# Kernel tuning notes

Measured on AMD Instinct MI355X. Metric: run time of the kernel, lower is better.

## Reference

```python
import jax, jax.numpy as jnp
import numpy as np

B, T, K = 64, 2000, 256
BLANK_LOGPROB = -1.0
NEG = jnp.float32(-1e30)  # stand-in for -inf, safe under logaddexp


def setup_inputs() -> dict:
    key = jax.random.key(0)
    k1, k2, k3 = jax.random.split(key, 3)
    attn_logprob = jax.random.normal(k1, (B, 1, T, K), dtype=jnp.float32)
    key_lens = jax.random.randint(k2, (B,), K // 2, K + 1)
    query_lens = jax.random.randint(k3, (B,), T // 2, T + 1)
    return {"attn_logprob": attn_logprob, "key_lens": key_lens, "query_lens": query_lens}


def _forward_sum(attn_logprob, key_lens, query_lens):
    # attn_logprob: [B, 1, T, K]; targets are 1..K_b (strictly increasing, all distinct)
    Bn, _, Tn, Kn = attn_logprob.shape
    logp = attn_logprob[:, 0]                                   # [B, T, K]
    # pad blank class at key index 0 (torch F.pad(pad=(1,0), value=blank_logprob))
    padded = jnp.pad(logp, ((0, 0), (0, 0), (1, 0)), constant_values=BLANK_LOGPROB)  # [B,T,K+1]
    # masked log_softmax over classes 0..K_b (matches per-sample slice [:key_lens+1])
    key_idx = jnp.arange(Kn + 1)
    key_mask = key_idx[None, :] <= key_lens[:, None]            # [B, K+1]
    masked = jnp.where(key_mask[:, None, :], padded, NEG)
    log_probs = jax.nn.log_softmax(masked, axis=-1)             # [B, T, K+1]

    # CTC forward DP. States s = 0..2K: even -> blank (class 0), odd -> label (s+1)//2.
    S = 2 * Kn + 1
    s_idx = jnp.arange(S)
    lab = jnp.where(s_idx % 2 == 0, 0, (s_idx + 1) // 2)        # class index per state
    # skip transition s-2 -> s allowed for odd s >= 3 (all labels distinct)
    skip_ok = (s_idx % 2 == 1) & (s_idx >= 3)

    emit0 = log_probs[:, 0, :][:, lab]                          # [B, S]
    alpha0 = jnp.full((Bn, S), NEG, dtype=log_probs.dtype)
    alpha0 = alpha0.at[:, 0].set(emit0[:, 0]).at[:, 1].set(emit0[:, 1])

    xs = jnp.moveaxis(log_probs[:, 1:, :], 1, 0)                # [T-1, B, K+1]
    ts = jnp.arange(1, Tn)

    def step(alpha, inp):
        x, t = inp
        emit = x[:, lab]                                        # [B, S]
        sh1 = jnp.concatenate([jnp.full((Bn, 1), NEG, alpha.dtype), alpha[:, :-1]], axis=1)
        sh2 = jnp.concatenate([jnp.full((Bn, 2), NEG, alpha.dtype), alpha[:, :-2]], axis=1)
        sh2 = jnp.where(skip_ok[None, :], sh2, NEG)
        new = jnp.logaddexp(jnp.logaddexp(alpha, sh1), sh2) + emit
        # freeze alpha once t >= query_lens[b] so final carry = alpha at t = T_b - 1
        return jnp.where((t < query_lens)[:, None], new, alpha), None

    alpha_final, _ = jax.lax.scan(step, alpha0, (xs, ts))       # [B, S]

    last = 2 * key_lens                                          # final state index per sample
    a_last = jnp.take_along_axis(alpha_final, last[:, None], axis=1)[:, 0]
    a_prev = jnp.take_along_axis(alpha_final, (last - 1)[:, None], axis=1)[:, 0]
    nll = -jnp.logaddexp(a_last, a_prev)                         # per-sample CTC NLL
    # torch CTCLoss(reduction='mean') on a batch of 1: divide by target length
    loss = nll / jnp.maximum(key_lens, 1).astype(nll.dtype)
    loss = jnp.where(nll > 0.5e30, 0.0, loss)                    # zero_infinity
    return jnp.mean(loss)


def reference(attn_logprob, key_lens, query_lens):
    return _forward_sum(attn_logprob, key_lens, query_lens)
```

## Files before the change

### kernel.cpp

```cpp
#include <hip/hip_runtime.h>
#include <cstdint>
#include <cstddef>

#define BB    64
#define TB    2000
#define KB    256

constexpr float LOG2E = 1.4426950408889634f;
constexpr float LN2f  = 0.6931471805599453f;
constexpr float WBF   = 0.36787944117144233f;

__device__ __forceinline__ float exp2i(int k) {
  return __uint_as_float((uint32_t)(127 + k) << 23);
}
__device__ __forceinline__ float shr1z(float v) {
  return __int_as_float(__builtin_amdgcn_update_dpp(
      0, __float_as_int(v), 0x138, 0xF, 0xF, true));
}
__device__ __forceinline__ float dmax64(float v) {
#define DSTEP(ctrl, rm, bc)                                                  \
  { float t = __int_as_float(__builtin_amdgcn_update_dpp(                    \
        __float_as_int(v), __float_as_int(v), (ctrl), (rm), 0xF, (bc)));     \
    v = fmaxf(v, t); }
  DSTEP(0x111, 0xF, true) DSTEP(0x112, 0xF, true) DSTEP(0x114, 0xF, true)
  DSTEP(0x118, 0xF, true) DSTEP(0x142, 0xA, false) DSTEP(0x143, 0xC, false)
#undef DSTEP
  return __int_as_float(__builtin_amdgcn_readlane(__float_as_int(v), 63));
}
__device__ __forceinline__ float dsum64(float v) {
#define DSTEP(ctrl, rm, bc)                                                  \
  { float t = __int_as_float(__builtin_amdgcn_update_dpp(                    \
        __float_as_int(v), __float_as_int(v), (ctrl), (rm), 0xF, (bc)));     \
    v += t; }
  DSTEP(0x111, 0xF, true) DSTEP(0x112, 0xF, true) DSTEP(0x114, 0xF, true)
  DSTEP(0x118, 0xF, true) DSTEP(0x142, 0xA, false) DSTEP(0x143, 0xC, false)
#undef DSTEP
  return v;
}
__device__ __forceinline__ float wsum64(float v) {
#pragma unroll
  for (int m = 32; m >= 1; m >>= 1) v += __shfl_xor(v, m, 64);
  return v;
}

__global__ __launch_bounds__(256, 1)
void fsl_main(const float* __restrict__ x, const int* __restrict__ key_lens,
              const int* __restrict__ query_lens, float* __restrict__ partial,
              float* __restrict__ alast, float* __restrict__ aprev) {
  __shared__ __align__(16) char ring[65536];
  __shared__ __align__(16) int prodG[4];
  __shared__ int consG;

  const int tid  = threadIdx.x;
  const int b    = blockIdx.x;
  const int lane = tid & 63;
  const int w    = tid >> 6;
  const int kl   = key_lens[b];
  const int qlen = query_lens[b];
  const int total = qlen - 1;
  const int ng    = (total + 7) >> 3;
  const float* xb  = x + (size_t)b * (TB * KB);
  const char*  xbc = (const char*)xb;
  const int lane16 = lane << 4;

  if (tid == 0) { prodG[0] = 0; prodG[1] = 0; prodG[2] = 0; prodG[3] = 0x7fffffff; consG = 0; }
  __syncthreads();

  if (w == 0) {
    float a0 = 0.f, a1 = 0.f, a2 = 0.f, a3 = 0.f;
    float b0 = 0.f, b1 = 0.f, b2 = 0.f, b3 = 0.f, s512 = 0.f;
    if (lane == 0) { a0 = WBF; b0 = __builtin_amdgcn_exp2f(xb[0] * LOG2E); }
    int Cw = 0;
    float m_red = dmax64(fmaxf(a0, b0));

    float4 e0, e1, e2, e3, e4, e5, e6, e7;
    float4 f0, f1, f2, f3, f4, f5, f6, f7;
    float4 g0, g1, g2, g3, g4, g5, g6, g7;

#define POLL(GN) do {                                                        \
    const int tgt_ = (GN);                                                   \
    for (;;) {                                                               \
      __asm__ __volatile__("" ::: "memory");                                 \
      const int4 fl_ = *(const int4*)prodG;                                  \
      if (min(fl_.x, min(fl_.y, fl_.z)) >= tgt_) break;                      \
      __builtin_amdgcn_s_sleep(1);                                           \
    }                                                                        \
    __asm__ __volatile__("" ::: "memory");                                   \
  } while (0)

#define LD8(E, g) do {                                                       \
    const char* sb_ = ring + (((g) & 7) << 13) + lane16;                     \
    E##0 = *(const float4*)(sb_);                                            \
    E##1 = *(const float4*)(sb_ + 1024);                                     \
    E##2 = *(const float4*)(sb_ + 2048);                                     \
    E##3 = *(const float4*)(sb_ + 3072);                                     \
    E##4 = *(const float4*)(sb_ + 4096);                                     \
    E##5 = *(const float4*)(sb_ + 5120);                                     \
    E##6 = *(const float4*)(sb_ + 6144);                                     \
    E##7 = *(const float4*)(sb_ + 7168);                                     \
  } while (0)

#define STEP1(EV) do {                                                       \
    const float pm1 = shr1z(b3);                                             \
    const float t0_ = a0 + pm1;                                              \
    const float t1_ = a1 + b0;                                               \
    const float t2_ = a2 + b1;                                               \
    const float t3_ = a3 + b2;                                               \
    s512 = s512 + b3;                                                        \
    b0 = (b0 + t0_) * EV.x;                                                  \
    b1 = (b1 + t1_) * EV.y;                                                  \
    b2 = (b2 + t2_) * EV.z;                                                  \
    b3 = (b3 + t3_) * EV.w;                                                  \
    a0 = t0_; a1 = t1_; a2 = t2_; a3 = t3_;                                  \
  } while (0)

#define STEP1G(EV, J) do { if ((J) < rem_) { STEP1(EV); } } while (0)

#define RUN8(E)  do { STEP1(E##0); STEP1(E##1); STEP1(E##2); STEP1(E##3);    \
                      STEP1(E##4); STEP1(E##5); STEP1(E##6); STEP1(E##7); } while (0)
#define RUN8G(E, RM) do { const int rem_ = (RM);                             \
                      STEP1G(E##0,0); STEP1G(E##1,1); STEP1G(E##2,2);        \
                      STEP1G(E##3,3); STEP1G(E##4,4); STEP1G(E##5,5);        \
                      STEP1G(E##6,6); STEP1G(E##7,7); } while (0)

#define APPLY() do {                                                         \
    int e_ = (int)((__float_as_uint(m_red) >> 23) & 0xFF) - 127;             \
    if (!(m_red > 0.f)) e_ = -24;                                            \
    const int k_ = e_ + 24;                      \
    if (k_ > 126) {                                                          \
      const int kh_ = k_ >> 1;                                               \
      const float s1_ = exp2i(-kh_), s2_ = exp2i(-(k_ - kh_));               \
      a0 *= s1_; a1 *= s1_; a2 *= s1_; a3 *= s1_;                            \
      b0 *= s1_; b1 *= s1_; b2 *= s1_; b3 *= s1_; s512 *= s1_;               \
      a0 *= s2_; a1 *= s2_; a2 *= s2_; a3 *= s2_;                            \
      b0 *= s2_; b1 *= s2_; b2 *= s2_; b3 *= s2_; s512 *= s2_;               \
    } else {                                                                 \
      const float s_ = exp2i(-k_);                                           \
      a0 *= s_; a1 *= s_; a2 *= s_; a3 *= s_;                                \
      b0 *= s_; b1 *= s_; b2 *= s_; b3 *= s_; s512 *= s_;                    \
    }                                                                        \
    Cw += k_;                                                                \
  } while (0)

#define MEASURE() do {                                                       \
    float ml_ = fmaxf(fmaxf(fmaxf(a0, a1), fmaxf(a2, a3)),                   \
                      fmaxf(fmaxf(b0, b1), fmaxf(b2, b3)));                  \
    ml_ = fmaxf(ml_, s512);                                                  \
    m_red = dmax64(ml_);                                                     \
  } while (0)

#define RUNGRP(E, G) do {                                                    \
    if (8 * (G) + 8 <= total) { RUN8(E); }                                   \
    else { RUN8G(E, total - 8 * (G)); }                                      \
    APPLY(); MEASURE();                                                      \
  } while (0)

    POLL(3);
    LD8(e, 0);
    if (1 < ng) LD8(f, 1);
    if (2 < ng) LD8(g, 2);
    int cg = 0;
    while (cg + 6 <= ng && 8 * (cg + 3) <= total) {
      POLL(cg + 6);
      RUN8(e); APPLY(); MEASURE(); LD8(e, cg + 3);
      RUN8(f); APPLY(); MEASURE(); LD8(f, cg + 4);
      RUN8(g); APPLY(); MEASURE(); LD8(g, cg + 5);
      __asm__ __volatile__("" ::: "memory");
      if (lane == 0) *(volatile int*)&consG = cg + 6;
      cg += 3;
    }
    for (; cg < ng; cg += 3) {
      POLL(min(cg + 6, ng));
      RUNGRP(e, cg);
      if (cg + 3 < ng) LD8(e, cg + 3);
      if (cg + 1 < ng) {
        RUNGRP(f, cg + 1);
        if (cg + 4 < ng) LD8(f, cg + 4);
      }
      if (cg + 2 < ng) {
        RUNGRP(g, cg + 2);
        if (cg + 5 < ng) LD8(g, cg + 5);
      }
      __asm__ __volatile__("" ::: "memory");
      if (lane == 0) *(volatile int*)&consG = cg + 6;
    }
#undef POLL
#undef LD8
#undef STEP1
#undef STEP1G
#undef RUN8
#undef RUN8G
#undef APPLY
#undef MEASURE
#undef RUNGRP

    float* ev = (float*)ring;
    float* od = (float*)(ring + 4096);
    *(float4*)(ev + (lane << 2)) = make_float4(a0, a1, a2, a3);
    *(float4*)(od + (lane << 2)) = make_float4(b0, b1, b2, b3);
    if (lane == 63) *(float*)(ring + 8192) = s512;
    __asm__ __volatile__("" ::: "memory");
    if (lane == 0) {
      const float aL = (kl < 256) ? ev[kl] : *(float*)(ring + 8192);
      const float aP = od[kl - 1];
      const float dC = (float)Cw - (float)total * LOG2E;
      alast[b] = (log2f(aL) + dC) * LN2f;
      aprev[b] = (log2f(aP) + dC) * LN2f;
    }
  } else {
    const int pw = w - 1;
    const int c0 = lane << 2;
    const float bs0 = (c0 + 0 < kl) ? LOG2E : -20000.f;
    const float bs1 = (c0 + 1 < kl) ? LOG2E : -20000.f;
    const float bs2 = (c0 + 2 < kl) ? LOG2E : -20000.f;
    const float bs3 = (c0 + 3 < kl) ? LOG2E : -20000.f;
    volatile int* vc = &consG;
    float acc = 0.f;

    if (pw == 0) {
      const float4 v = *(const float4*)(xbc + lane16);
      float s_ = __builtin_amdgcn_exp2f(fmaf(v.x, LOG2E, bs0))
               + __builtin_amdgcn_exp2f(fmaf(v.y, LOG2E, bs1))
               + __builtin_amdgcn_exp2f(fmaf(v.z, LOG2E, bs2))
               + __builtin_amdgcn_exp2f(fmaf(v.w, LOG2E, bs3));
      s_ = dsum64(s_);
      acc += __builtin_amdgcn_logf((s_ + 1.0f) * WBF);
    }

    float4 A0, A1, A2, A3, A4, A5, A6, A7;
    float4 B0, B1, B2, B3, B4, B5, B6, B7;
    float4 C0, C1, C2, C3, C4, C5, C6, C7;

#define LOADG(P, GG) do {                                                    \
    const int rb_ = 8 * (GG) + 1;                                            \
    P##0 = *(const float4*)(xbc + (size_t)min(rb_ + 0, TB - 1) * 1024 + lane16); \
    P##1 = *(const float4*)(xbc + (size_t)min(rb_ + 1, TB - 1) * 1024 + lane16); \
    P##2 = *(const float4*)(xbc + (size_t)min(rb_ + 2, TB - 1) * 1024 + lane16); \
    P##3 = *(const float4*)(xbc + (size_t)min(rb_ + 3, TB - 1) * 1024 + lane16); \
    P##4 = *(const float4*)(xbc + (size_t)min(rb_ + 4, TB - 1) * 1024 + lane16); \
    P##5 = *(const float4*)(xbc + (size_t)min(rb_ + 5, TB - 1) * 1024 + lane16); \
    P##6 = *(const float4*)(xbc + (size_t)min(rb_ + 6, TB - 1) * 1024 + lane16); \
    P##7 = *(const float4*)(xbc + (size_t)min(rb_ + 7, TB - 1) * 1024 + lane16); \
  } while (0)

#define PR1(V, J) do {                                                       \
    float4 wv_;                                                              \
    wv_.x = __builtin_amdgcn_exp2f(fmaf(V.x, LOG2E, bs0));                   \
    wv_.y = __builtin_amdgcn_exp2f(fmaf(V.y, LOG2E, bs1));                   \
    wv_.z = __builtin_amdgcn_exp2f(fmaf(V.z, LOG2E, bs2));                   \
    wv_.w = __builtin_amdgcn_exp2f(fmaf(V.w, LOG2E, bs3));                   \
    *(float4*)(dstb_ + ((J) << 10)) = wv_;                                   \
    if (rb_ + (J) <= total) {                                                \
      float sr_ = (wv_.x + wv_.y) + (wv_.z + wv_.w);                         \
      sr_ = dsum64(sr_);                                                     \
      acc += __builtin_amdgcn_logf((sr_ + 1.0f) * WBF);                      \
    }                                                                        \
  } while (0)

#define PROC(P, GG) do {                                                     \
    const int rb_ = 8 * (GG) + 1;                                            \
    if ((GG) >= 8) {                                    \
      int c_ = *vc;                                                          \
      while (c_ < (GG) - 7) { __builtin_amdgcn_s_sleep(2); c_ = *vc; }       \
      __asm__ __volatile__("" ::: "memory");                                 \
    }                                                                        \
    char* dstb_ = ring + (((GG) & 7) << 13) + lane16;                        \
    PR1(P##0, 0); PR1(P##1, 1); PR1(P##2, 2); PR1(P##3, 3);                  \
    PR1(P##4, 4); PR1(P##5, 5); PR1(P##6, 6); PR1(P##7, 7);                  \
    __asm__ __volatile__("s_waitcnt lgkmcnt(0)" ::: "memory");               \
    if (lane == 0) *(volatile int*)&prodG[pw] = (GG) + 3;                    \
  } while (0)

    LOADG(A, pw); LOADG(B, pw + 3);
    int g = pw;
    for (;;) {
      LOADG(C, g + 6);
      PROC(A, g);
      g += 3; if (g >= ng) break;
      LOADG(A, g + 6);
      PROC(B, g);
      g += 3; if (g >= ng) break;
      LOADG(B, g + 6);
      PROC(C, g);
      g += 3; if (g >= ng) break;
    }
#undef LOADG
#undef PR1
#undef PROC
    __asm__ __volatile__("" ::: "memory");
    if (lane == 0) *(volatile int*)&prodG[pw] = 0x7fffffff;
    if (lane == 63) partial[4 * b + pw] = acc;
  }
}

__global__ __launch_bounds__(64)
void fsl_finish(const float* __restrict__ partial, const int* __restrict__ key_lens,
                const float* __restrict__ alast, const float* __restrict__ aprev,
                float* __restrict__ out) {
  const int b = threadIdx.x;
  const float SumLse =
      ((partial[4 * b] + partial[4 * b + 1]) + partial[4 * b + 2]) * LN2f;
  const float al = alast[b], ap = aprev[b];
  const float mx = fmaxf(al, ap);
  const float lae = (mx == -INFINITY) ? -INFINITY
                                      : mx + log1pf(expf(-fabsf(al - ap)));
  const float nll = SumLse - lae;
  const int kl = key_lens[b];
  float lv = nll / (float)max(kl, 1);
  if (nll > 5e29f) lv = 0.f;
  float v = wsum64(lv);
  if (b == 0) out[0] = v * (1.0f / 64.0f);
}

extern "C" void kernel_launch(void* const* d_in, const int* in_sizes, int n_in,
                              void* d_out, int out_size, void* d_ws, size_t ws_size,
                              hipStream_t stream) {
  const float* x     = (const float*)d_in[0];
  const int*   klens = (const int*)d_in[1];
  const int*   qlens = (const int*)d_in[2];
  float* out = (float*)d_out;

  float* partial = (float*)d_ws;
  float* alast   = partial + BB * 4;
  float* aprev   = alast + BB;

  fsl_main  <<<BB, 256, 0, stream>>>(x, klens, qlens, partial, alast, aprev);
  fsl_finish<<<1, 64, 0, stream>>>(partial, klens, alast, aprev, out);
}
```

Measured before the change: 119.7 us.

## Offload per-row log-sum-exp to separate blocks, freeing producer warps for DP feed

Moves the per-timestep log-sum-exp normalizer computation out of the producer warps in the 64 DP blocks and into 2000 extra blocks. Each extra warp handles 16 rows of one sample. The finish kernel now reduces 125 partials per sample. Producer warps only do exp and the LDS write, which shortens the critical path feeding the serial DP warp. The change also removes the sleep in the consumer poll loop and enlarges the shared ring declaration. The extra blocks re-read the whole input from HBM and compete for CUs with the 64 DP blocks; the larger LDS allocation may also limit co-residency.

```diff
diff --git a/kernel.cpp b/kernel.cpp
--- a/kernel.cpp
+++ b/kernel.cpp
@@ -5,6 +5,9 @@
 #define BB    64
 #define TB    2000
 #define KB    256
+#define WPB   125
+#define RPW   16
+#define NLSEB 2000
 
 constexpr float LOG2E = 1.4426950408889634f;
 constexpr float LN2f  = 0.6931471805599453f;
@@ -43,39 +46,44 @@
   return v;
 }
 
+typedef const __attribute__((address_space(1))) unsigned int* gas1p;
+typedef __attribute__((address_space(3))) unsigned int* las3p;
+
 __global__ __launch_bounds__(256, 1)
 void fsl_main(const float* __restrict__ x, const int* __restrict__ key_lens,
               const int* __restrict__ query_lens, float* __restrict__ partial,
               float* __restrict__ alast, float* __restrict__ aprev) {
-  __shared__ __align__(16) char ring[65536];
+  __shared__ __align__(16) char ring[86016];
   __shared__ __align__(16) int prodG[4];
   __shared__ int consG;
 
   const int tid  = threadIdx.x;
-  const int b    = blockIdx.x;
   const int lane = tid & 63;
   const int w    = tid >> 6;
-  const int kl   = key_lens[b];
-  const int qlen = query_lens[b];
-  const int total = qlen - 1;
-  const int ng    = (total + 7) >> 3;
-  const float* xb  = x + (size_t)b * (TB * KB);
-  const char*  xbc = (const char*)xb;
-  const int lane16 = lane << 4;
-
-  if (tid == 0) { prodG[0] = 0; prodG[1] = 0; prodG[2] = 0; prodG[3] = 0x7fffffff; consG = 0; }
-  __syncthreads();
-
-  if (w == 0) {
-    float a0 = 0.f, a1 = 0.f, a2 = 0.f, a3 = 0.f;
-    float b0 = 0.f, b1 = 0.f, b2 = 0.f, b3 = 0.f, s512 = 0.f;
-    if (lane == 0) { a0 = WBF; b0 = __builtin_amdgcn_exp2f(xb[0] * LOG2E); }
-    int Cw = 0;
-    float m_red = dmax64(fmaxf(a0, b0));
-
-    float4 e0, e1, e2, e3, e4, e5, e6, e7;
-    float4 f0, f1, f2, f3, f4, f5, f6, f7;
-    float4 g0, g1, g2, g3, g4, g5, g6, g7;
+
+  if (blockIdx.x < BB) {
+    const int b    = blockIdx.x;
+    const int kl   = key_lens[b];
+    const int qlen = query_lens[b];
+    const int total = qlen - 1;
+    const int ng    = (total + 7) >> 3;
+    const float* xb  = x + (size_t)b * (TB * KB);
+    const char*  xbc = (const char*)xb;
+    const int lane16 = lane << 4;
+
+    if (tid == 0) { prodG[0] = 0; prodG[1] = 0; prodG[2] = 0; prodG[3] = 0x7fffffff; consG = 0; }
+    __syncthreads();
+
+    if (w == 0) {
+      float a0 = 0.f, a1 = 0.f, a2 = 0.f, a3 = 0.f;
+      float b0 = 0.f, b1 = 0.f, b2 = 0.f, b3 = 0.f, s512 = 0.f;
+      if (lane == 0) { a0 = WBF; b0 = __builtin_amdgcn_exp2f(xb[0] * LOG2E); }
+      int Cw = 0;
+      float m_red = dmax64(fmaxf(a0, b0));
+
+      float4 e0, e1, e2, e3, e4, e5, e6, e7;
+      float4 f0, f1, f2, f3, f4, f5, f6, f7;
+      float4 g0, g1, g2, g3, g4, g5, g6, g7;
 
 #define POLL(GN) do {                                                        \
     const int tgt_ = (GN);                                                   \
@@ -83,7 +91,6 @@
       __asm__ __volatile__("" ::: "memory");                                 \
       const int4 fl_ = *(const int4*)prodG;                                  \
       if (min(fl_.x, min(fl_.y, fl_.z)) >= tgt_) break;                      \
-      __builtin_amdgcn_s_sleep(1);                                           \
     }                                                                        \
     __asm__ __volatile__("" ::: "memory");                                   \
   } while (0)
@@ -155,35 +162,35 @@
     APPLY(); MEASURE();                                                      \
   } while (0)
 
-    POLL(3);
-    LD8(e, 0);
-    if (1 < ng) LD8(f, 1);
-    if (2 < ng) LD8(g, 2);
-    int cg = 0;
-    while (cg + 6 <= ng && 8 * (cg + 3) <= total) {
-      POLL(cg + 6);
-      RUN8(e); APPLY(); MEASURE(); LD8(e, cg + 3);
-      RUN8(f); APPLY(); MEASURE(); LD8(f, cg + 4);
-      RUN8(g); APPLY(); MEASURE(); LD8(g, cg + 5);
-      __asm__ __volatile__("" ::: "memory");
-      if (lane == 0) *(volatile int*)&consG = cg + 6;
-      cg += 3;
-    }
-    for (; cg < ng; cg += 3) {
-      POLL(min(cg + 6, ng));
-      RUNGRP(e, cg);
-      if (cg + 3 < ng) LD8(e, cg + 3);
-      if (cg + 1 < ng) {
-        RUNGRP(f, cg + 1);
-        if (cg + 4 < ng) LD8(f, cg + 4);
+      POLL(3);
+      LD8(e, 0);
+      if (1 < ng) LD8(f, 1);
+      if (2 < ng) LD8(g, 2);
+      int cg = 0;
+      while (cg + 6 <= ng && 8 * (cg + 3) <= total) {
+        POLL(cg + 6);
+        RUN8(e); APPLY(); MEASURE(); LD8(e, cg + 3);
+        RUN8(f); APPLY(); MEASURE(); LD8(f, cg + 4);
+        RUN8(g); APPLY(); MEASURE(); LD8(g, cg + 5);
+        __asm__ __volatile__("" ::: "memory");
+        if (lane == 0) *(volatile int*)&consG = cg + 6;
+        cg += 3;
       }
-      if (cg + 2 < ng) {
-        RUNGRP(g, cg + 2);
-        if (cg + 5 < ng) LD8(g, cg + 5);
+      for (; cg < ng; cg += 3) {
+        POLL(min(cg + 6, ng));
+        RUNGRP(e, cg);
+        if (cg + 3 < ng) LD8(e, cg + 3);
+        if (cg + 1 < ng) {
+          RUNGRP(f, cg + 1);
+          if (cg + 4 < ng) LD8(f, cg + 4);
+        }
+        if (cg + 2 < ng) {
+          RUNGRP(g, cg + 2);
+          if (cg + 5 < ng) LD8(g, cg + 5);
+        }
+        __asm__ __volatile__("" ::: "memory");
+        if (lane == 0) *(volatile int*)&consG = cg + 6;
       }
-      __asm__ __volatile__("" ::: "memory");
-      if (lane == 0) *(volatile int*)&consG = cg + 6;
-    }
 #undef POLL
 #undef LD8
 #undef STEP1
@@ -194,42 +201,31 @@
 #undef MEASURE
 #undef RUNGRP
 
-    float* ev = (float*)ring;
-    float* od = (float*)(ring + 4096);
-    *(float4*)(ev + (lane << 2)) = make_float4(a0, a1, a2, a3);
-    *(float4*)(od + (lane << 2)) = make_float4(b0, b1, b2, b3);
-    if (lane == 63) *(float*)(ring + 8192) = s512;
-    __asm__ __volatile__("" ::: "memory");
-    if (lane == 0) {
-      const float aL = (kl < 256) ? ev[kl] : *(float*)(ring + 8192);
-      const float aP = od[kl - 1];
-      const float dC = (float)Cw - (float)total * LOG2E;
-      alast[b] = (log2f(aL) + dC) * LN2f;
-      aprev[b] = (log2f(aP) + dC) * LN2f;
-    }
-  } else {
-    const int pw = w - 1;
-    const int c0 = lane << 2;
-    const float bs0 = (c0 + 0 < kl) ? LOG2E : -20000.f;
-    const float bs1 = (c0 + 1 < kl) ? LOG2E : -20000.f;
-    const float bs2 = (c0 + 2 < kl) ? LOG2E : -20000.f;
-    const float bs3 = (c0 + 3 < kl) ? LOG2E : -20000.f;
-    volatile int* vc = &consG;
-    float acc = 0.f;
-
-    if (pw == 0) {
-      const float4 v = *(const float4*)(xbc + lane16);
-      float s_ = __builtin_amdgcn_exp2f(fmaf(v.x, LOG2E, bs0))
-               + __builtin_amdgcn_exp2f(fmaf(v.y, LOG2E, bs1))
-               + __builtin_amdgcn_exp2f(fmaf(v.z, LOG2E, bs2))
-               + __builtin_amdgcn_exp2f(fmaf(v.w, LOG2E, bs3));
-      s_ = dsum64(s_);
-      acc += __builtin_amdgcn_logf((s_ + 1.0f) * WBF);
-    }
-
-    float4 A0, A1, A2, A3, A4, A5, A6, A7;
-    float4 B0, B1, B2, B3, B4, B5, B6, B7;
-    float4 C0, C1, C2, C3, C4, C5, C6, C7;
+      float* ev = (float*)ring;
+      float* od = (float*)(ring + 4096);
+      *(float4*)(ev + (lane << 2)) = make_float4(a0, a1, a2, a3);
+      *(float4*)(od + (lane << 2)) = make_float4(b0, b1, b2, b3);
+      if (lane == 63) *(float*)(ring + 8192) = s512;
+      __asm__ __volatile__("" ::: "memory");
+      if (lane == 0) {
+        const float aL = (kl < 256) ? ev[kl] : *(float*)(ring + 8192);
+        const float aP = od[kl - 1];
+        const float dC = (float)Cw - (float)total * LOG2E;
+        alast[b] = (log2f(aL) + dC) * LN2f;
+        aprev[b] = (log2f(aP) + dC) * LN2f;
+      }
+    } else {
+      const int pw = w - 1;
+      const int c0 = lane << 2;
+      const float bs0 = (c0 + 0 < kl) ? LOG2E : -20000.f;
+      const float bs1 = (c0 + 1 < kl) ? LOG2E : -20000.f;
+      const float bs2 = (c0 + 2 < kl) ? LOG2E : -20000.f;
+      const float bs3 = (c0 + 3 < kl) ? LOG2E : -20000.f;
+      volatile int* vc = &consG;
+
+      float4 A0, A1, A2, A3, A4, A5, A6, A7;
+      float4 B0, B1, B2, B3, B4, B5, B6, B7;
+      float4 C0, C1, C2, C3, C4, C5, C6, C7;
 
 #define LOADG(P, GG) do {                                                    \
     const int rb_ = 8 * (GG) + 1;                                            \
@@ -250,15 +246,9 @@
     wv_.z = __builtin_amdgcn_exp2f(fmaf(V.z, LOG2E, bs2));                   \
     wv_.w = __builtin_amdgcn_exp2f(fmaf(V.w, LOG2E, bs3));                   \
     *(float4*)(dstb_ + ((J) << 10)) = wv_;                                   \
-    if (rb_ + (J) <= total) {                                                \
-      float sr_ = (wv_.x + wv_.y) + (wv_.z + wv_.w);                         \
-      sr_ = dsum64(sr_);                                                     \
-      acc += __builtin_amdgcn_logf((sr_ + 1.0f) * WBF);                      \
-    }                                                                        \
   } while (0)
 
 #define PROC(P, GG) do {                                                     \
-    const int rb_ = 8 * (GG) + 1;                                            \
     if ((GG) >= 8) {                                    \
       int c_ = *vc;                                                          \
       while (c_ < (GG) - 7) { __builtin_amdgcn_s_sleep(2); c_ = *vc; }       \
@@ -271,45 +261,85 @@
     if (lane == 0) *(volatile int*)&prodG[pw] = (GG) + 3;                    \
   } while (0)
 
-    LOADG(A, pw); LOADG(B, pw + 3);
-    int g = pw;
-    for (;;) {
-      LOADG(C, g + 6);
-      PROC(A, g);
-      g += 3; if (g >= ng) break;
-      LOADG(A, g + 6);
-      PROC(B, g);
-      g += 3; if (g >= ng) break;
-      LOADG(B, g + 6);
-      PROC(C, g);
-      g += 3; if (g >= ng) break;
-    }
+      LOADG(A, pw); LOADG(B, pw + 3);
+      int g = pw;
+      for (;;) {
+        LOADG(C, g + 6);
+        PROC(A, g);
+        g += 3; if (g >= ng) break;
+        LOADG(A, g + 6);
+        PROC(B, g);
+        g += 3; if (g >= ng) break;
+        LOADG(B, g + 6);
+        PROC(C, g);
+        g += 3; if (g >= ng) break;
+      }
 #undef LOADG
 #undef PR1
 #undef PROC
-    __asm__ __volatile__("" ::: "memory");
-    if (lane == 0) *(volatile int*)&prodG[pw] = 0x7fffffff;
-    if (lane == 63) partial[4 * b + pw] = acc;
+      __asm__ __volatile__("" ::: "memory");
+      if (lane == 0) *(volatile int*)&prodG[pw] = 0x7fffffff;
+    }
+
+  } else {
+    const int gwid = (blockIdx.x - BB) * 4 + w;
+    const int b    = gwid / WPB;
+    const int widx = gwid - b * WPB;
+    const int kl   = key_lens[b];
+    const int qlen = query_lens[b];
+    const float* xb = x + (size_t)b * (TB * KB);
+    const int c0 = lane * 4;
+    const float bA = (c0 + 0 < kl) ? 0.f : -20000.f;
+    const float bBv= (c0 + 1 < kl) ? 0.f : -20000.f;
+    const float bC = (c0 + 2 < kl) ? 0.f : -20000.f;
+    const float bD = (c0 + 3 < kl) ? 0.f : -20000.f;
+    float acc = 0.f;
+    const int tbase = widx * RPW;
+#pragma unroll 4
+    for (int k = 0; k < RPW; ++k) {
+      const int t = tbase + k;
+      const float4 v = *(const float4*)(xb + (size_t)t * KB + c0);
+      float s = __builtin_amdgcn_exp2f(fmaf(v.x, LOG2E, bA))
+              + __builtin_amdgcn_exp2f(fmaf(v.y, LOG2E, bBv))
+              + __builtin_amdgcn_exp2f(fmaf(v.z, LOG2E, bC))
+              + __builtin_amdgcn_exp2f(fmaf(v.w, LOG2E, bD));
+      s = dsum64(s);
+      s += WBF;
+      const float l2 = __builtin_amdgcn_logf(s);
+      acc += (t < qlen) ? l2 : 0.f;
+    }
+    if (lane == 63) partial[gwid] = acc * LN2f;
   }
 }
 
-__global__ __launch_bounds__(64)
+__global__ __launch_bounds__(256)
 void fsl_finish(const float* __restrict__ partial, const int* __restrict__ key_lens,
                 const float* __restrict__ alast, const float* __restrict__ aprev,
                 float* __restrict__ out) {
-  const int b = threadIdx.x;
-  const float SumLse =
-      ((partial[4 * b] + partial[4 * b + 1]) + partial[4 * b + 2]) * LN2f;
-  const float al = alast[b], ap = aprev[b];
-  const float mx = fmaxf(al, ap);
-  const float lae = (mx == -INFINITY) ? -INFINITY
-                                      : mx + log1pf(expf(-fabsf(al - ap)));
-  const float nll = SumLse - lae;
-  const int kl = key_lens[b];
-  float lv = nll / (float)max(kl, 1);
-  if (nll > 5e29f) lv = 0.f;
-  float v = wsum64(lv);
-  if (b == 0) out[0] = v * (1.0f / 64.0f);
+  const int tid = threadIdx.x;
+  const int b = tid >> 2, q = tid & 3;
+  float s = 0.f;
+  for (int j = q; j < WPB; j += 4) s += partial[b * WPB + j];
+  s += __shfl_xor(s, 1, 64);
+  s += __shfl_xor(s, 2, 64);
+  float lossb = 0.f;
+  if (q == 0) {
+    const float SumLse = s;
+    const float al = alast[b], ap = aprev[b];
+    const float mx = fmaxf(al, ap);
+    const float lae = (mx == -INFINITY) ? -INFINITY
+                                        : mx + log1pf(expf(-fabsf(al - ap)));
+    const float nll = SumLse - lae;
+    const int kl = key_lens[b];
+    float lv = nll / (float)max(kl, 1);
+    if (nll > 5e29f) lv = 0.f;
+    lossb = lv;
+  }
+  float v = wsum64(lossb);
+  __shared__ float sm[4];
+  if ((tid & 63) == 0) sm[tid >> 6] = v;
+  __syncthreads();
+  if (tid == 0) out[0] = ((sm[0] + sm[1]) + (sm[2] + sm[3])) * (1.0f / 64.0f);
 }
 
 extern "C" void kernel_launch(void* const* d_in, const int* in_sizes, int n_in,
@@ -321,9 +351,9 @@
   float* out = (float*)d_out;
 
   float* partial = (float*)d_ws;
-  float* alast   = partial + BB * 4;
+  float* alast   = partial + BB * WPB;
   float* aprev   = alast + BB;
 
-  fsl_main  <<<BB, 256, 0, stream>>>(x, klens, qlens, partial, alast, aprev);
-  fsl_finish<<<1, 64, 0, stream>>>(partial, klens, alast, aprev, out);
-}
+  fsl_main  <<<BB + NLSEB, 256, 0, stream>>>(x, klens, qlens, partial, alast, aprev);
+  fsl_finish<<<1, 256, 0, stream>>>(partial, klens, alast, aprev, out);
+}
```

Measured after the change: 121.1 us. About the same (+1.1%).
